# Kernel optimization log

Measured on AMD Instinct MI355X. Metric: run time of the kernel, lower is better.

The kernel has to match this reference:

```python
import jax, jax.numpy as jnp
import numpy as np

SINKHORN_ITERS = 10


def _optimal_transport(attn, phi, iters):
    # attn: [N,H,W,W], phi: scalar dustbin score
    bs, h, w, _ = attn.shape
    marginal = jnp.concatenate([jnp.ones((w,), attn.dtype), jnp.array([float(w)], attn.dtype)]) / (2.0 * w)
    log_mu = jnp.log(marginal)  # [W+1], broadcasts over [N,H,W+1]
    log_nu = log_mu
    # augment with dustbin row/col filled with phi -> [N,H,W+1,W+1]
    sim = jnp.concatenate([attn, jnp.broadcast_to(phi, (bs, h, w, 1))], axis=-1)
    sim = jnp.concatenate([sim, jnp.broadcast_to(phi, (bs, h, 1, w + 1))], axis=-2)

    def body(i, uv):
        u, v = uv
        v = log_nu - jax.nn.logsumexp(sim + u[..., :, None], axis=2)
        u = log_mu - jax.nn.logsumexp(sim + v[..., None, :], axis=3)
        return (u, v)

    u0 = jnp.zeros((bs, h, w + 1), attn.dtype)
    u, v = jax.lax.fori_loop(0, iters, body, (u0, u0))
    attn_ot = sim + u[..., :, None] + v[..., None, :]
    return jnp.exp(attn_ot + jnp.log(2.0 * w))


def _compute_low_res_disp(pos_shift, attn, occ_mask=None):
    # attn: [N,H,W,W] (dustbins removed); pos_shift: [W,W]
    w = attn.shape[-1]
    high_response = jnp.argmax(attn, axis=-1)  # [N,H,W]
    response_range = jnp.stack([high_response - 1, high_response, high_response + 1], axis=-1)  # [N,H,W,3]
    attn_pad = jnp.pad(attn, ((0, 0), (0, 0), (0, 0), (1, 1)))
    attn_rw = jnp.take_along_axis(attn_pad, response_range + 1, axis=-1)  # [N,H,W,3]
    norm = attn_rw.sum(-1, keepdims=True)
    norm = jnp.where(norm < 0.1, 1.0, norm)  # occ_mask is None branch
    attn_rw = attn_rw / norm
    pos_pad = jnp.pad(pos_shift, ((0, 0), (1, 1)))  # [W,W+2]
    pos_pad = jnp.broadcast_to(pos_pad[None, None], attn_pad.shape)
    pos_rw = jnp.take_along_axis(pos_pad, response_range + 1, axis=-1)
    disp = (attn_rw * pos_rw).sum(-1)  # [N,H,W]
    return disp, norm


def setup_inputs() -> dict:
    key = jax.random.key(0)
    k1, _ = jax.random.split(key)
    N, H, W = 4, 120, 256
    attn_weight = jax.random.normal(k1, (N, H, W, W), dtype=jnp.float32)
    phi = jnp.zeros((1,), dtype=jnp.float32)
    return {"attn_weight": attn_weight, "phi": phi}


def reference(attn_weight, phi):
    w = attn_weight.shape[2]
    attn_ot = _optimal_transport(attn_weight, phi[0], SINKHORN_ITERS)  # [N,H,W+1,W+1]
    # relative position shift, clamped at 0
    pos = jnp.arange(w, dtype=attn_weight.dtype)
    pos_shift = jnp.maximum(pos[:, None] - pos[None, :], 0.0)  # [W,W]
    disp_pred_low_res, matched_attn = _compute_low_res_disp(pos_shift, attn_ot[..., :-1, :-1], None)
    occ_pred = 1.0 - matched_attn.squeeze(-1)  # [N,H,W]
    return disp_pred_low_res, occ_pred
```

## Files before the change

kernel.cpp:

```cpp
#include <hip/hip_runtime.h>
#include <cstdint>

namespace {

constexpr int W = 256;
constexpr int ITERS = 10;
constexpr int PSTR = 260;

template <int CTRL>
__device__ __forceinline__ float dpp_add(float x) {
  int y = __builtin_amdgcn_mov_dpp(__float_as_int(x), CTRL, 0xF, 0xF, true);
  return x + __int_as_float(y);
}
template <int PAT>
__device__ __forceinline__ float swz_add(float x) {
  return x + __int_as_float(__builtin_amdgcn_ds_swizzle(__float_as_int(x), PAT));
}
__device__ __forceinline__ float allred32(float x) {
  x = dpp_add<0xB1>(x);
  x = dpp_add<0x4E>(x);
  x = dpp_add<0x141>(x);
  x = dpp_add<0x140>(x);
  x = swz_add<0x401F>(x);
  return x;
}
__device__ __forceinline__ float rcpf(float x) {
  float r;
  asm("v_rcp_f32 %0, %1" : "=v"(r) : "v"(x));
  return r;
}

__global__ __launch_bounds__(512)
__attribute__((amdgpu_waves_per_eu(2, 2)))
void sinkhorn_disp_kernel(
    const float* __restrict__ attn,
    const float* __restrict__ phi_p,
    float* __restrict__ out,
    int nh)
{
  __shared__ __align__(16) float fpart[8][PSTR];
  __shared__ __align__(16) float ev_l[W];
  __shared__ __align__(16) float seup[16];

  const int tid  = threadIdx.x;
  const int lane = tid & 63;
  const int wid  = tid >> 6;
  const int cg   = lane & 31;
  const int rg   = 2 * wid + (lane >> 5);
  const int bid  = blockIdx.x;

  const int ch0 = 4 * ((2 * cg) ^ ((cg >> 2) & 7));

  const float ephi = __int_as_float(
      __builtin_amdgcn_readfirstlane(__float_as_int(__expf(phi_p[0]))));
  const float inv2w = 1.0f / (2.0f * W);

  float Er[16][8];
  {
    const float* src = attn + (size_t)bid * (W * W)
                     + (size_t)(rg * 16) * W + cg * 8;
    #pragma unroll
    for (int r = 0; r < 16; ++r) {
      float4 x0 = *(const float4*)(src + r * W);
      float4 x1 = *(const float4*)(src + r * W + 4);
      Er[r][0] = __expf(x0.x); Er[r][1] = __expf(x0.y);
      Er[r][2] = __expf(x0.z); Er[r][3] = __expf(x0.w);
      Er[r][4] = __expf(x1.x); Er[r][5] = __expf(x1.y);
      Er[r][6] = __expf(x1.z); Er[r][7] = __expf(x1.w);
    }
  }

  float eul[16];
  #pragma unroll
  for (int r = 0; r < 16; ++r) eul[r] = 1.0f;
  float euW  = 1.0f;
  float evWk = 0.0f;

  const bool  do_pf = (bid + 256 < nh);
  const float* pfp  = attn + (size_t)(bid + 256) * (W * W) + (size_t)tid * 16;
  float pfv = 0.0f;

  for (int it = 0; it < ITERS; ++it) {
    if (do_pf && it < 8)
      pfv = pfp[(size_t)it * (512 * 16)];
    {
      float cp[8];
      #pragma unroll
      for (int b = 0; b < 8; ++b) cp[b] = 0.0f;
      #pragma unroll
      for (int r = 0; r < 16; ++r) {
        float u = eul[r];
        #pragma unroll
        for (int b = 0; b < 8; ++b)
          cp[b] = __builtin_fmaf(Er[r][b], u, cp[b]);
      }
      #pragma unroll
      for (int b = 0; b < 8; ++b) cp[b] += __shfl_xor(cp[b], 32, 64);
      if (lane < 32) {
        *(float4*)&fpart[wid][ch0    ] = make_float4(cp[0], cp[1], cp[2], cp[3]);
        *(float4*)&fpart[wid][ch0 ^ 4] = make_float4(cp[4], cp[5], cp[6], cp[7]);
      }
      if ((lane & 31) == 0) {
        float s = (((eul[0] + eul[1]) + (eul[2] + eul[3]))
                 + ((eul[4] + eul[5]) + (eul[6] + eul[7])))
                + (((eul[8] + eul[9]) + (eul[10] + eul[11]))
                 + ((eul[12] + eul[13]) + (eul[14] + eul[15])));
        seup[rg] = s;
      }
    }
    __syncthreads();
    {
      const int j  = tid >> 1;
      const int fj = ((((j >> 2) ^ ((j >> 5) & 7)) << 2) | (j & 3));
      const int g0 = (tid & 1) * 4;
      float s = (fpart[g0][fj] + fpart[g0 + 1][fj])
              + (fpart[g0 + 2][fj] + fpart[g0 + 3][fj]);
      s = dpp_add<0xB1>(s);
      if (!(tid & 1)) ev_l[fj] = inv2w * rcpf(s + ephi * euW);
      float4 s0 = *(const float4*)&seup[0];
      float4 s1 = *(const float4*)&seup[4];
      float4 s2 = *(const float4*)&seup[8];
      float4 s3 = *(const float4*)&seup[12];
      float Seu = ((((s0.x + s0.y) + (s0.z + s0.w))
                  + ((s1.x + s1.y) + (s1.z + s1.w)))
                 + (((s2.x + s2.y) + (s2.z + s2.w))
                  + ((s3.x + s3.y) + (s3.z + s3.w))));
      evWk = 0.5f * rcpf(ephi * (Seu + euW));
    }
    __syncthreads();
    {
      float4 v0 = *(const float4*)&ev_l[ch0];
      float4 v1 = *(const float4*)&ev_l[ch0 ^ 4];
      float vl[8] = {v0.x, v0.y, v0.z, v0.w, v1.x, v1.y, v1.z, v1.w};
      float rp[16];
      #pragma unroll
      for (int r = 0; r < 16; ++r) {
        float s = 0.0f;
        #pragma unroll
        for (int b = 0; b < 8; ++b)
          s = __builtin_fmaf(Er[r][b], vl[b], s);
        rp[r] = s;
      }
      float sev = ((vl[0] + vl[1]) + (vl[2] + vl[3]))
                + ((vl[4] + vl[5]) + (vl[6] + vl[7]));
      #pragma unroll
      for (int r = 0; r < 16; ++r) rp[r] = allred32(rp[r]);
      sev = allred32(sev);
      const float eAdd = ephi * evWk;
      #pragma unroll
      for (int r = 0; r < 16; ++r) eul[r] = inv2w * rcpf(rp[r] + eAdd);
      euW = 0.5f * rcpf(ephi * (sev + evWk));
    }
    if (do_pf && it < 8) asm volatile("" :: "v"(pfv));
  }

  float vl[8];
  {
    float4 v0 = *(const float4*)&ev_l[ch0];
    float4 v1 = *(const float4*)&ev_l[ch0 ^ 4];
    vl[0] = v0.x; vl[1] = v0.y; vl[2] = v0.z; vl[3] = v0.w;
    vl[4] = v1.x; vl[5] = v1.y; vl[6] = v1.z; vl[7] = v1.w;
  }
  float res_disp = 0.0f, res_occ = 0.0f;
  #pragma unroll
  for (int r = 0; r < 16; ++r) {
    float v[8];
    #pragma unroll
    for (int b = 0; b < 8; ++b) v[b] = Er[r][b] * vl[b];
    float m = v[0]; int mj = cg * 8;
    #pragma unroll
    for (int b = 1; b < 8; ++b) {
      if (v[b] > m) { m = v[b]; mj = cg * 8 + b; }
    }
    unsigned long long best =
        (((unsigned long long)__float_as_uint(m)) << 32) |
        (unsigned)(65535 - mj);
    #pragma unroll
    for (int off = 16; off > 0; off >>= 1) {
      unsigned long long o = __shfl_xor(best, off, 32);
      if (o > best) best = o;
    }
    const int jm = 65535 - (int)(best & 0xffffffffull);
    const int i  = rg * 16 + r;
    const float us = eul[r] * (2.0f * W);
    float num = 0.0f, den = 0.0f;
    #pragma unroll
    for (int b = 0; b < 8; ++b) {
      int j = cg * 8 + b;
      if (j >= jm - 1 && j <= jm + 1) {
        float wv = v[b] * us;
        den += wv;
        num += wv * fmaxf((float)(i - j), 0.0f);
      }
    }
    den = allred32(den);
    num = allred32(num);
    if (cg == r) {
      float norm = (den < 0.1f) ? 1.0f : den;
      res_disp = num / norm;
      res_occ  = 1.0f - norm;
    }
  }
  if (cg < 16) {
    const int i = rg * 16 + cg;
    out[(size_t)bid * W + i] = res_disp;
    out[(size_t)nh * W + (size_t)bid * W + i] = res_occ;
  }
}

}

extern "C" void kernel_launch(void* const* d_in, const int* in_sizes, int n_in,
                              void* d_out, int out_size, void* d_ws, size_t ws_size,
                              hipStream_t stream) {
  (void)n_in; (void)d_ws; (void)ws_size; (void)out_size;
  const float* attn = (const float*)d_in[0];
  const float* phi  = (const float*)d_in[1];
  float* out = (float*)d_out;
  const int nh = in_sizes[0] / (W * W);
  sinkhorn_disp_kernel<<<dim3(nh), dim3(512), 0, stream>>>(attn, phi, out, nh);
}
```

Measured before the change: 226.4 us.

## Spill a quarter of exp-attention tile to LDS to double occupancy

Four of the sixteen rows of exponentiated attention that each thread keeps in registers now live in a swizzled per-thread LDS region. The row scaling vector u moves to shared memory as well. This cuts VGPR use enough to raise waves_per_eu from 2 to 4, so two blocks can share a CU and hide each other's latency. The next-block prefetch is removed. In exchange, the LDS rows must be re-read in every Sinkhorn half-step, u updates go through LDS with lane selects, and about 73KB of LDS per block limits how many blocks fit.

```diff
diff --git a/kernel.cpp b/kernel.cpp
--- a/kernel.cpp
+++ b/kernel.cpp
@@ -31,15 +31,17 @@
 }
 
 __global__ __launch_bounds__(512)
-__attribute__((amdgpu_waves_per_eu(2, 2)))
+__attribute__((amdgpu_waves_per_eu(4, 4)))
 void sinkhorn_disp_kernel(
     const float* __restrict__ attn,
     const float* __restrict__ phi_p,
     float* __restrict__ out,
     int nh)
 {
+  __shared__ __align__(16) float E_lds[512 * 32];
   __shared__ __align__(16) float fpart[8][PSTR];
   __shared__ __align__(16) float ev_l[W];
+  __shared__ __align__(16) float eul_l[W];
   __shared__ __align__(16) float seup[16];
 
   const int tid  = threadIdx.x;
@@ -48,6 +50,9 @@
   const int cg   = lane & 31;
   const int rg   = 2 * wid + (lane >> 5);
   const int bid  = blockIdx.x;
+  const int sw   = tid & 7;
+  float* myE = &E_lds[tid * 32];
+  #define RDCH(c) (*(const float4*)&myE[4 * ((c) ^ sw)])
 
   const int ch0 = 4 * ((2 * cg) ^ ((cg >> 2) & 7));
 
@@ -55,12 +60,12 @@
       __builtin_amdgcn_readfirstlane(__float_as_int(__expf(phi_p[0]))));
   const float inv2w = 1.0f / (2.0f * W);
 
-  float Er[16][8];
+  float Er[12][8];
   {
     const float* src = attn + (size_t)bid * (W * W)
                      + (size_t)(rg * 16) * W + cg * 8;
     #pragma unroll
-    for (int r = 0; r < 16; ++r) {
+    for (int r = 0; r < 12; ++r) {
       float4 x0 = *(const float4*)(src + r * W);
       float4 x1 = *(const float4*)(src + r * W + 4);
       Er[r][0] = __expf(x0.x); Er[r][1] = __expf(x0.y);
@@ -68,31 +73,55 @@
       Er[r][4] = __expf(x1.x); Er[r][5] = __expf(x1.y);
       Er[r][6] = __expf(x1.z); Er[r][7] = __expf(x1.w);
     }
-  }
-
-  float eul[16];
-  #pragma unroll
-  for (int r = 0; r < 16; ++r) eul[r] = 1.0f;
+    #pragma unroll
+    for (int r = 0; r < 4; ++r) {
+      float4 x0 = *(const float4*)(src + (12 + r) * W);
+      float4 x1 = *(const float4*)(src + (12 + r) * W + 4);
+      *(float4*)&myE[4 * ((2 * r)     ^ sw)] =
+          make_float4(__expf(x0.x), __expf(x0.y), __expf(x0.z), __expf(x0.w));
+      *(float4*)&myE[4 * ((2 * r + 1) ^ sw)] =
+          make_float4(__expf(x1.x), __expf(x1.y), __expf(x1.z), __expf(x1.w));
+    }
+  }
+  if (cg < 16) eul_l[16 * rg + cg] = 1.0f;
   float euW  = 1.0f;
   float evWk = 0.0f;
 
-  const bool  do_pf = (bid + 256 < nh);
-  const float* pfp  = attn + (size_t)(bid + 256) * (W * W) + (size_t)tid * 16;
-  float pfv = 0.0f;
-
   for (int it = 0; it < ITERS; ++it) {
-    if (do_pf && it < 8)
-      pfv = pfp[(size_t)it * (512 * 16)];
     {
       float cp[8];
       #pragma unroll
       for (int b = 0; b < 8; ++b) cp[b] = 0.0f;
-      #pragma unroll
-      for (int r = 0; r < 16; ++r) {
-        float u = eul[r];
-        #pragma unroll
-        for (int b = 0; b < 8; ++b)
-          cp[b] = __builtin_fmaf(Er[r][b], u, cp[b]);
+      float sSeu = 0.0f;
+      #pragma unroll
+      for (int q = 0; q < 3; ++q) {
+        float4 u4 = *(const float4*)&eul_l[16 * rg + 4 * q];
+        sSeu += ((u4.x + u4.y) + (u4.z + u4.w));
+        float uu[4] = {u4.x, u4.y, u4.z, u4.w};
+        #pragma unroll
+        for (int k = 0; k < 4; ++k) {
+          #pragma unroll
+          for (int b = 0; b < 8; ++b)
+            cp[b] = __builtin_fmaf(Er[4 * q + k][b], uu[k], cp[b]);
+        }
+      }
+      {
+        float4 u4 = *(const float4*)&eul_l[16 * rg + 12];
+        sSeu += ((u4.x + u4.y) + (u4.z + u4.w));
+        float uu[4] = {u4.x, u4.y, u4.z, u4.w};
+        #pragma unroll
+        for (int r = 0; r < 4; ++r) {
+          float4 e0 = RDCH(2 * r), e1 = RDCH(2 * r + 1);
+          float ua = uu[r];
+          cp[0] = __builtin_fmaf(e0.x, ua, cp[0]);
+          cp[1] = __builtin_fmaf(e0.y, ua, cp[1]);
+          cp[2] = __builtin_fmaf(e0.z, ua, cp[2]);
+          cp[3] = __builtin_fmaf(e0.w, ua, cp[3]);
+          cp[4] = __builtin_fmaf(e1.x, ua, cp[4]);
+          cp[5] = __builtin_fmaf(e1.y, ua, cp[5]);
+          cp[6] = __builtin_fmaf(e1.z, ua, cp[6]);
+          cp[7] = __builtin_fmaf(e1.w, ua, cp[7]);
+        }
       }
       #pragma unroll
       for (int b = 0; b < 8; ++b) cp[b] += __shfl_xor(cp[b], 32, 64);
@@ -100,13 +129,7 @@
         *(float4*)&fpart[wid][ch0    ] = make_float4(cp[0], cp[1], cp[2], cp[3]);
         *(float4*)&fpart[wid][ch0 ^ 4] = make_float4(cp[4], cp[5], cp[6], cp[7]);
       }
-      if ((lane & 31) == 0) {
-        float s = (((eul[0] + eul[1]) + (eul[2] + eul[3]))
-                 + ((eul[4] + eul[5]) + (eul[6] + eul[7])))
-                + (((eul[8] + eul[9]) + (eul[10] + eul[11]))
-                 + ((eul[12] + eul[13]) + (eul[14] + eul[15])));
-        seup[rg] = s;
-      }
+      if ((lane & 31) == 0) seup[rg] = sSeu;
     }
     __syncthreads();
     {
@@ -132,26 +155,47 @@
       float4 v0 = *(const float4*)&ev_l[ch0];
       float4 v1 = *(const float4*)&ev_l[ch0 ^ 4];
       float vl[8] = {v0.x, v0.y, v0.z, v0.w, v1.x, v1.y, v1.z, v1.w};
-      float rp[16];
-      #pragma unroll
-      for (int r = 0; r < 16; ++r) {
-        float s = 0.0f;
-        #pragma unroll
-        for (int b = 0; b < 8; ++b)
-          s = __builtin_fmaf(Er[r][b], vl[b], s);
-        rp[r] = s;
+      const float eAdd = ephi * evWk;
+      #pragma unroll
+      for (int q = 0; q < 3; ++q) {
+        float rp[4];
+        #pragma unroll
+        for (int k = 0; k < 4; ++k) {
+          float s = 0.0f;
+          #pragma unroll
+          for (int b = 0; b < 8; ++b)
+            s = __builtin_fmaf(Er[4 * q + k][b], vl[b], s);
+          rp[k] = s;
+        }
+        #pragma unroll
+        for (int k = 0; k < 4; ++k) rp[k] = allred32(rp[k]);
+        float wv = rp[0];
+        wv = (cg == 1) ? rp[1] : wv;
+        wv = (cg == 2) ? rp[2] : wv;
+        wv = (cg == 3) ? rp[3] : wv;
+        if (cg < 4) eul_l[16 * rg + 4 * q + cg] = inv2w * rcpf(wv + eAdd);
+      }
+      {
+        float rp[4];
+        #pragma unroll
+        for (int r = 0; r < 4; ++r) {
+          float4 e0 = RDCH(2 * r), e1 = RDCH(2 * r + 1);
+          rp[r] = e0.x * vl[0] + e0.y * vl[1] + e0.z * vl[2] + e0.w * vl[3]
+                + e1.x * vl[4] + e1.y * vl[5] + e1.z * vl[6] + e1.w * vl[7];
+        }
+        #pragma unroll
+        for (int k = 0; k < 4; ++k) rp[k] = allred32(rp[k]);
+        float wv = rp[0];
+        wv = (cg == 1) ? rp[1] : wv;
+        wv = (cg == 2) ? rp[2] : wv;
+        wv = (cg == 3) ? rp[3] : wv;
+        if (cg < 4) eul_l[16 * rg + 12 + cg] = inv2w * rcpf(wv + eAdd);
       }
       float sev = ((vl[0] + vl[1]) + (vl[2] + vl[3]))
                 + ((vl[4] + vl[5]) + (vl[6] + vl[7]));
-      #pragma unroll
-      for (int r = 0; r < 16; ++r) rp[r] = allred32(rp[r]);
       sev = allred32(sev);
-      const float eAdd = ephi * evWk;
-      #pragma unroll
-      for (int r = 0; r < 16; ++r) eul[r] = inv2w * rcpf(rp[r] + eAdd);
       euW = 0.5f * rcpf(ephi * (sev + evWk));
     }
-    if (do_pf && it < 8) asm volatile("" :: "v"(pfv));
   }
 
   float vl[8];
@@ -165,8 +209,16 @@
   #pragma unroll
   for (int r = 0; r < 16; ++r) {
     float v[8];
-    #pragma unroll
-    for (int b = 0; b < 8; ++b) v[b] = Er[r][b] * vl[b];
+    if (r < 12) {
+      #pragma unroll
+      for (int b = 0; b < 8; ++b) v[b] = Er[r < 12 ? r : 0][b] * vl[b];
+    } else {
+      float4 e0 = RDCH(2 * (r - 12)), e1 = RDCH(2 * (r - 12) + 1);
+      v[0] = e0.x * vl[0]; v[1] = e0.y * vl[1];
+      v[2] = e0.z * vl[2]; v[3] = e0.w * vl[3];
+      v[4] = e1.x * vl[4]; v[5] = e1.y * vl[5];
+      v[6] = e1.z * vl[6]; v[7] = e1.w * vl[7];
+    }
     float m = v[0]; int mj = cg * 8;
     #pragma unroll
     for (int b = 1; b < 8; ++b) {
@@ -182,7 +234,7 @@
     }
     const int jm = 65535 - (int)(best & 0xffffffffull);
     const int i  = rg * 16 + r;
-    const float us = eul[r] * (2.0f * W);
+    const float us = eul_l[i] * (2.0f * W);
     float num = 0.0f, den = 0.0f;
     #pragma unroll
     for (int b = 0; b < 8; ++b) {
@@ -206,6 +258,7 @@
     out[(size_t)bid * W + i] = res_disp;
     out[(size_t)nh * W + (size_t)bid * W + i] = res_occ;
   }
+  #undef RDCH
 }
 
 }
```

Result: slower. 256.9 us (+13.5%).

## Double-buffer column partials and compute v redundantly per thread to drop a barrier

Applied to the files above, without the earlier changes.

Each thread now reads all eight warp partial sums for its own eight columns straight from shared memory and computes the column scaling v locally. This removes the shared ev_l buffer and one __syncthreads per Sinkhorn iteration. The partial and seup buffers are double-buffered by iteration parity so the next iteration's writes cannot race with the current reads. In exchange each thread does more LDS reads (16 float4 instead of 4 scalars) and redundant reciprocals, which raises LDS traffic and register pressure.

```diff
diff --git a/kernel.cpp b/kernel.cpp
--- a/kernel.cpp
+++ b/kernel.cpp
@@ -28,6 +28,9 @@
   float r;
   asm("v_rcp_f32 %0, %1" : "=v"(r) : "v"(x));
   return r;
+}
+__device__ __forceinline__ float4 f4add(float4 a, float4 b) {
+  return make_float4(a.x + b.x, a.y + b.y, a.z + b.z, a.w + b.w);
 }
 
 __global__ __launch_bounds__(512)
@@ -38,9 +41,8 @@
     float* __restrict__ out,
     int nh)
 {
-  __shared__ __align__(16) float fpart[8][PSTR];
-  __shared__ __align__(16) float ev_l[W];
-  __shared__ __align__(16) float seup[16];
+  __shared__ __align__(16) float fpart[2][8][PSTR];
+  __shared__ __align__(16) float seup[2][16];
 
   const int tid  = threadIdx.x;
   const int lane = tid & 63;
@@ -73,14 +75,17 @@
   float eul[16];
   #pragma unroll
   for (int r = 0; r < 16; ++r) eul[r] = 1.0f;
-  float euW  = 1.0f;
-  float evWk = 0.0f;
+  float euW = 1.0f;
+  float vl[8];
+  #pragma unroll
+  for (int b = 0; b < 8; ++b) vl[b] = 0.0f;
 
   const bool  do_pf = (bid + 256 < nh);
   const float* pfp  = attn + (size_t)(bid + 256) * (W * W) + (size_t)tid * 16;
   float pfv = 0.0f;
 
   for (int it = 0; it < ITERS; ++it) {
+    const int p = it & 1;
     if (do_pf && it < 8)
       pfv = pfp[(size_t)it * (512 * 16)];
     {
@@ -97,41 +102,57 @@
       #pragma unroll
       for (int b = 0; b < 8; ++b) cp[b] += __shfl_xor(cp[b], 32, 64);
       if (lane < 32) {
-        *(float4*)&fpart[wid][ch0    ] = make_float4(cp[0], cp[1], cp[2], cp[3]);
-        *(float4*)&fpart[wid][ch0 ^ 4] = make_float4(cp[4], cp[5], cp[6], cp[7]);
+        *(float4*)&fpart[p][wid][ch0    ] = make_float4(cp[0], cp[1], cp[2], cp[3]);
+        *(float4*)&fpart[p][wid][ch0 ^ 4] = make_float4(cp[4], cp[5], cp[6], cp[7]);
       }
       if ((lane & 31) == 0) {
         float s = (((eul[0] + eul[1]) + (eul[2] + eul[3]))
                  + ((eul[4] + eul[5]) + (eul[6] + eul[7])))
                 + (((eul[8] + eul[9]) + (eul[10] + eul[11]))
                  + ((eul[12] + eul[13]) + (eul[14] + eul[15])));
-        seup[rg] = s;
+        seup[p][rg] = s;
       }
     }
     __syncthreads();
     {
-      const int j  = tid >> 1;
-      const int fj = ((((j >> 2) ^ ((j >> 5) & 7)) << 2) | (j & 3));
-      const int g0 = (tid & 1) * 4;
-      float s = (fpart[g0][fj] + fpart[g0 + 1][fj])
-              + (fpart[g0 + 2][fj] + fpart[g0 + 3][fj]);
-      s = dpp_add<0xB1>(s);
-      if (!(tid & 1)) ev_l[fj] = inv2w * rcpf(s + ephi * euW);
-      float4 s0 = *(const float4*)&seup[0];
-      float4 s1 = *(const float4*)&seup[4];
-      float4 s2 = *(const float4*)&seup[8];
-      float4 s3 = *(const float4*)&seup[12];
+      float4 A0 = *(const float4*)&fpart[p][0][ch0];
+      float4 A1 = *(const float4*)&fpart[p][1][ch0];
+      float4 A2 = *(const float4*)&fpart[p][2][ch0];
+      float4 A3 = *(const float4*)&fpart[p][3][ch0];
+      float4 A4 = *(const float4*)&fpart[p][4][ch0];
+      float4 A5 = *(const float4*)&fpart[p][5][ch0];
+      float4 A6 = *(const float4*)&fpart[p][6][ch0];
+      float4 A7 = *(const float4*)&fpart[p][7][ch0];
+      float4 sa = f4add(f4add(f4add(A0, A1), f4add(A2, A3)),
+                        f4add(f4add(A4, A5), f4add(A6, A7)));
+      float4 B0 = *(const float4*)&fpart[p][0][ch0 ^ 4];
+      float4 B1 = *(const float4*)&fpart[p][1][ch0 ^ 4];
+      float4 B2 = *(const float4*)&fpart[p][2][ch0 ^ 4];
+      float4 B3 = *(const float4*)&fpart[p][3][ch0 ^ 4];
+      float4 B4 = *(const float4*)&fpart[p][4][ch0 ^ 4];
+      float4 B5 = *(const float4*)&fpart[p][5][ch0 ^ 4];
+      float4 B6 = *(const float4*)&fpart[p][6][ch0 ^ 4];
+      float4 B7 = *(const float4*)&fpart[p][7][ch0 ^ 4];
+      float4 sb = f4add(f4add(f4add(B0, B1), f4add(B2, B3)),
+                        f4add(f4add(B4, B5), f4add(B6, B7)));
+      float4 s0 = *(const float4*)&seup[p][0];
+      float4 s1 = *(const float4*)&seup[p][4];
+      float4 s2 = *(const float4*)&seup[p][8];
+      float4 s3 = *(const float4*)&seup[p][12];
       float Seu = ((((s0.x + s0.y) + (s0.z + s0.w))
                   + ((s1.x + s1.y) + (s1.z + s1.w)))
                  + (((s2.x + s2.y) + (s2.z + s2.w))
                   + ((s3.x + s3.y) + (s3.z + s3.w))));
-      evWk = 0.5f * rcpf(ephi * (Seu + euW));
-    }
-    __syncthreads();
-    {
-      float4 v0 = *(const float4*)&ev_l[ch0];
-      float4 v1 = *(const float4*)&ev_l[ch0 ^ 4];
-      float vl[8] = {v0.x, v0.y, v0.z, v0.w, v1.x, v1.y, v1.z, v1.w};
+      const float evW = 0.5f * rcpf(ephi * (Seu + euW));
+      const float eW  = ephi * euW;
+      vl[0] = inv2w * rcpf(sa.x + eW);
+      vl[1] = inv2w * rcpf(sa.y + eW);
+      vl[2] = inv2w * rcpf(sa.z + eW);
+      vl[3] = inv2w * rcpf(sa.w + eW);
+      vl[4] = inv2w * rcpf(sb.x + eW);
+      vl[5] = inv2w * rcpf(sb.y + eW);
+      vl[6] = inv2w * rcpf(sb.z + eW);
+      vl[7] = inv2w * rcpf(sb.w + eW);
       float rp[16];
       #pragma unroll
       for (int r = 0; r < 16; ++r) {
@@ -146,21 +167,14 @@
       #pragma unroll
       for (int r = 0; r < 16; ++r) rp[r] = allred32(rp[r]);
       sev = allred32(sev);
-      const float eAdd = ephi * evWk;
+      const float eAdd = ephi * evW;
       #pragma unroll
       for (int r = 0; r < 16; ++r) eul[r] = inv2w * rcpf(rp[r] + eAdd);
-      euW = 0.5f * rcpf(ephi * (sev + evWk));
+      euW = 0.5f * rcpf(ephi * (sev + evW));
     }
     if (do_pf && it < 8) asm volatile("" :: "v"(pfv));
   }
 
-  float vl[8];
-  {
-    float4 v0 = *(const float4*)&ev_l[ch0];
-    float4 v1 = *(const float4*)&ev_l[ch0 ^ 4];
-    vl[0] = v0.x; vl[1] = v0.y; vl[2] = v0.z; vl[3] = v0.w;
-    vl[4] = v1.x; vl[5] = v1.y; vl[6] = v1.z; vl[7] = v1.w;
-  }
   float res_disp = 0.0f, res_occ = 0.0f;
   #pragma unroll
   for (int r = 0; r < 16; ++r) {
```

Measured after the change: 234.8 us. +3.7%, slower.
